# Kernel tuning notes

Measured on AMD Instinct MI355X. Metric: run time of the kernel, lower is better.

Reference implementation:

```python
import jax, jax.numpy as jnp
import numpy as np

B, S, D, H = 4, 8192, 512, 8
HD = D // H  # head_dim = 64


def setup_inputs() -> dict:
    key0 = jax.random.key(0)
    ks = jax.random.split(key0, 8)
    scale_in = (2.0 / (D + 3 * D)) ** 0.5  # xavier_uniform-ish std
    scale_out = (2.0 / (D + D)) ** 0.5
    return {
        "query": jax.random.normal(ks[0], (B, S, D), dtype=jnp.float32),
        "key": jax.random.normal(ks[1], (B, S, D), dtype=jnp.float32),
        "value": jax.random.normal(ks[2], (B, S, D), dtype=jnp.float32),
        "key_padding_mask": jax.random.bernoulli(ks[3], 0.1, (B, S)),  # True = ignore
        "in_proj_weight": jax.random.normal(ks[4], (3 * D, D), dtype=jnp.float32) * scale_in,
        "in_proj_bias": jnp.zeros((3 * D,), dtype=jnp.float32),
        "out_proj_weight": jax.random.normal(ks[5], (D, D), dtype=jnp.float32) * scale_out,
        "out_proj_bias": jnp.zeros((D,), dtype=jnp.float32),
    }


def _phi(x):
    # ELU+1 feature map (strictly positive)
    return jax.nn.elu(x) + 1.0


def reference(query, key, value, key_padding_mask, in_proj_weight, in_proj_bias,
              out_proj_weight, out_proj_bias):
    # NB: the torch module projects q,k,v all from `query`; key/value args are unused.
    qkv = query @ in_proj_weight.T + in_proj_bias  # (B,S,3D)
    q, k, v = jnp.split(qkv, 3, axis=-1)
    # (B,S,D) -> (B,H,S,HD)
    def to_heads(x):
        return x.reshape(B, S, H, HD).transpose(0, 2, 1, 3)
    q = _phi(to_heads(q))
    k = _phi(to_heads(k))
    v = to_heads(v)
    mask = (~key_padding_mask).astype(q.dtype)[:, None, :, None]  # (B,1,S,1)
    k = k * mask
    v = v * mask
    kv = jnp.einsum('bhsd,bhse->bhde', k, v)          # (B,H,HD,HD)
    numerator = jnp.einsum('bhsd,bhde->bhse', q, kv)  # (B,H,S,HD)
    k_sum = k.sum(axis=2)                              # (B,H,HD)
    denominator = jnp.einsum('bhsd,bhd->bhs', q, k_sum)[..., None]
    denominator = jnp.maximum(denominator, 1e-6)
    attn_out = (numerator / denominator).transpose(0, 2, 1, 3).reshape(B, S, D)
    return attn_out @ out_proj_weight.T + out_proj_bias
```

## Files before the change

kernel.cpp:

```cpp
#include <hip/hip_runtime.h>
#include <cstddef>

#define B_   4
#define S_   8192
#define D_   512
#define H_   8
#define HD_  64
#define NROW (B_ * S_)
#define NQ   ((size_t)NROW * D_)

typedef __attribute__((ext_vector_type(4))) float  f32x4;
typedef __attribute__((ext_vector_type(8))) short  s16x8;
typedef __attribute__((ext_vector_type(4))) unsigned short u16x4;
typedef __attribute__((ext_vector_type(8))) unsigned short u16x8;

__device__ __forceinline__ float phi_f(float x) {
    return x > 0.0f ? x + 1.0f : expf(x);
}
__device__ __forceinline__ float bf2f(unsigned short u) {
    return __uint_as_float(((unsigned int)u) << 16);
}
__device__ __forceinline__ unsigned short f2bf(float f) {
    unsigned int u = __float_as_uint(f);
    u += 0x7fffu + ((u >> 16) & 1u);
    return (unsigned short)(u >> 16);
}

#define GLOBAL_AS(p) ((const __attribute__((address_space(1))) void*)(p))
#define LDS_AS(p)    ((__attribute__((address_space(3))) void*)(p))

__global__ void detect_mask(const unsigned char* __restrict__ m, int* __restrict__ flag) {
    __shared__ int sany;
    if (threadIdx.x == 0) sany = 0;
    __syncthreads();
    int any = 0;
    for (int i = 1 + 4 * (int)threadIdx.x; i < NROW; i += 4 * 256) any |= m[i];
    if (any) atomicOr(&sany, 1);
    __syncthreads();
    if (threadIdx.x == 0) *flag = sany ? 1 : 0;
}

__global__ __launch_bounds__(256) void convert_all(
    const float* __restrict__ q,  unsigned short* __restrict__ qb,
    const float* __restrict__ wi, unsigned short* __restrict__ wib,
    const float* __restrict__ wo, unsigned short* __restrict__ wob,
    const unsigned char* __restrict__ kpm, const int* __restrict__ flag,
    float* __restrict__ fmask)
{
    const size_t i = (size_t)blockIdx.x * 256 + threadIdx.x;
    {
        const float4 v = *(const float4*)&q[i * 4];
        u16x4 o; o.x = f2bf(v.x); o.y = f2bf(v.y); o.z = f2bf(v.z); o.w = f2bf(v.w);
        *(u16x4*)&qb[i * 4] = o;
    }
    if (i < 786432 / 4) {
        const float4 v = *(const float4*)&wi[i * 4];
        u16x4 o; o.x = f2bf(v.x); o.y = f2bf(v.y); o.z = f2bf(v.z); o.w = f2bf(v.w);
        *(u16x4*)&wib[i * 4] = o;
    }
    if (i < 262144 / 4) {
        const float4 v = *(const float4*)&wo[i * 4];
        u16x4 o; o.x = f2bf(v.x); o.y = f2bf(v.y); o.z = f2bf(v.z); o.w = f2bf(v.w);
        *(u16x4*)&wob[i * 4] = o;
    }
    if (i < NROW) {
        const bool ignore = (*flag) ? (kpm[i] != 0) : (((const int*)kpm)[i] != 0);
        fmask[i] = ignore ? 0.0f : 1.0f;
    }
}

__global__ __launch_bounds__(256) void gemm_mfma(
    const unsigned short* __restrict__ A,  int lda,
    const unsigned short* __restrict__ Bw, int ldb,
    const float* __restrict__ bias, int K, int mode,
    const float* __restrict__ fmask,
    unsigned short* __restrict__ Cq,
    unsigned short* __restrict__ Ck,
    unsigned short* __restrict__ Cv,
    float* __restrict__ Cout)
{
    __shared__ __align__(16) unsigned short As[128 * 32];
    __shared__ __align__(16) unsigned short Bs[128 * 32];
    __shared__ float fm[128];

    const int t    = threadIdx.x;
    const int lane = t & 63;
    const int wave = t >> 6;
    const int wm   = wave & 1;
    const int wn   = wave >> 1;

    const int nbx = gridDim.x;
    const int nwg = nbx * gridDim.y;
    int id = blockIdx.y * nbx + blockIdx.x;
    id = (id & 7) * (nwg >> 3) + (id >> 3);
    const int m0 = (id / nbx) * 128;
    const int n0 = (id % nbx) * 128;

    if (mode == 0 && t < 128) fm[t] = fmask[m0 + t];

    f32x4 acc[4][4] = {};

    const int sr = lane >> 2;
    const int sk = (lane & 3) * 8;

    for (int k0 = 0; k0 < K; k0 += 32) {
        __syncthreads();
        #pragma unroll
        for (int j = 0; j < 2; ++j) {
            const int row = wave * 32 + j * 16;
            const unsigned short* g = A + (size_t)(m0 + row + sr) * lda + k0 + sk;
            __builtin_amdgcn_global_load_lds(GLOBAL_AS(g), LDS_AS(&As[row * 32]), 16, 0, 0);
        }
        #pragma unroll
        for (int j = 0; j < 2; ++j) {
            const int row = wave * 32 + j * 16;
            const unsigned short* g = Bw + (size_t)(n0 + row + sr) * ldb + k0 + sk;
            __builtin_amdgcn_global_load_lds(GLOBAL_AS(g), LDS_AS(&Bs[row * 32]), 16, 0, 0);
        }
        __syncthreads();

        const int fr = lane & 15;
        const int fk = (lane >> 4) * 8;
        s16x8 af[4], bf[4];
        #pragma unroll
        for (int i = 0; i < 4; ++i)
            af[i] = *(const s16x8*)&As[(wm * 64 + i * 16 + fr) * 32 + fk];
        #pragma unroll
        for (int j = 0; j < 4; ++j)
            bf[j] = *(const s16x8*)&Bs[(wn * 64 + j * 16 + fr) * 32 + fk];
        #pragma unroll
        for (int i = 0; i < 4; ++i)
            #pragma unroll
            for (int j = 0; j < 4; ++j)
                acc[i][j] = __builtin_amdgcn_mfma_f32_16x16x32_bf16(af[i], bf[j], acc[i][j], 0, 0, 0);
    }

    const int col  = lane & 15;
    const int rowq = (lane >> 4) * 4;
    float bj[4];
    #pragma unroll
    for (int j = 0; j < 4; ++j) bj[j] = bias[n0 + wn * 64 + j * 16 + col];

    if (mode == 1) {
        #pragma unroll
        for (int i = 0; i < 4; ++i)
            #pragma unroll
            for (int r = 0; r < 4; ++r) {
                const int m = m0 + wm * 64 + i * 16 + rowq + r;
                #pragma unroll
                for (int j = 0; j < 4; ++j) {
                    const int n = n0 + wn * 64 + j * 16 + col;
                    Cout[(size_t)m * D_ + n] = acc[i][j][r] + bj[j];
                }
            }
    } else {
        const int region = n0 >> 9;
        unsigned short* Cb = region == 0 ? Cq : (region == 1 ? Ck : Cv);
        #pragma unroll
        for (int i = 0; i < 4; ++i)
            #pragma unroll
            for (int r = 0; r < 4; ++r) {
                const int ml = wm * 64 + i * 16 + rowq + r;
                const int m  = m0 + ml;
                const float mk = fm[ml];
                #pragma unroll
                for (int j = 0; j < 4; ++j) {
                    const int n  = (n0 & 511) + wn * 64 + j * 16 + col;
                    float v = acc[i][j][r] + bj[j];
                    if (region == 0)      v = phi_f(v);
                    else if (region == 1) v = phi_f(v) * mk;
                    else                  v = v * mk;
                    Cb[(size_t)m * D_ + n] = f2bf(v);
                }
            }
    }
}

__global__ __launch_bounds__(256) void kv_reduce(
    const unsigned short* __restrict__ kbuf,
    const unsigned short* __restrict__ vbuf,
    float* __restrict__ part_kv,
    float* __restrict__ part_ks)
{
    const int bh = blockIdx.x, chunk = blockIdx.y;
    const int b = bh >> 3, h = bh & 7;

    __shared__ __align__(16) float Ks[16][68];
    __shared__ __align__(16) float Vs[16][68];

    const int t    = threadIdx.x;
    const int wave = t >> 6;
    const int lane = t & 63;
    const int tx   = lane & 7;
    const int ty   = lane >> 3;

    const int sr = (t & 127) >> 3;
    const int sc = (t & 7) * 8;
    const unsigned short* src = (t < 128 ? kbuf : vbuf) + (size_t)b * S_ * D_ + h * HD_;
    float (*dst)[68] = (t < 128) ? Ks : Vs;

    float acc[8][8] = {};
    float ks[8] = {};
    const int s0 = chunk * (S_ / 16);

    for (int it = 0; it < S_ / 16; it += 16) {
        const size_t s = (size_t)(s0 + it + sr);
        const u16x8 x = *(const u16x8*)&src[s * D_ + sc];
        __syncthreads();
        float4 f0, f1;
        f0.x = bf2f(x[0]); f0.y = bf2f(x[1]); f0.z = bf2f(x[2]); f0.w = bf2f(x[3]);
        f1.x = bf2f(x[4]); f1.y = bf2f(x[5]); f1.z = bf2f(x[6]); f1.w = bf2f(x[7]);
        *(float4*)&dst[sr][sc]     = f0;
        *(float4*)&dst[sr][sc + 4] = f1;
        __syncthreads();
        #pragma unroll
        for (int ss0 = 0; ss0 < 4; ++ss0) {
            const int ss = wave + ss0 * 4;
            const float4 a0 = *(const float4*)&Ks[ss][ty * 8];
            const float4 a1 = *(const float4*)&Ks[ss][ty * 8 + 4];
            const float4 v0 = *(const float4*)&Vs[ss][tx * 8];
            const float4 v1 = *(const float4*)&Vs[ss][tx * 8 + 4];
            const float av[8] = {a0.x, a0.y, a0.z, a0.w, a1.x, a1.y, a1.z, a1.w};
            const float vv[8] = {v0.x, v0.y, v0.z, v0.w, v1.x, v1.y, v1.z, v1.w};
            #pragma unroll
            for (int i2 = 0; i2 < 8; ++i2)
                #pragma unroll
                for (int j2 = 0; j2 < 8; ++j2)
                    acc[i2][j2] += av[i2] * vv[j2];
            if (tx == 0) {
                #pragma unroll
                for (int i2 = 0; i2 < 8; ++i2) ks[i2] += av[i2];
            }
        }
    }

    const int p = bh * 64 + chunk * 4 + wave;
    float* pk = part_kv + (size_t)p * 4096;
    #pragma unroll
    for (int i2 = 0; i2 < 8; ++i2) {
        #pragma unroll
        for (int j4 = 0; j4 < 2; ++j4) {
            float4 o;
            o.x = acc[i2][j4 * 4 + 0]; o.y = acc[i2][j4 * 4 + 1];
            o.z = acc[i2][j4 * 4 + 2]; o.w = acc[i2][j4 * 4 + 3];
            *(float4*)&pk[(ty * 8 + i2) * 64 + tx * 8 + j4 * 4] = o;
        }
    }
    if (tx == 0) {
        float* ps = part_ks + (size_t)p * 64;
        #pragma unroll
        for (int i2 = 0; i2 < 8; ++i2) ps[ty * 8 + i2] = ks[i2];
    }
}

__global__ void kv_reduce2(const float* __restrict__ part_kv,
                           const float* __restrict__ part_ks,
                           unsigned short* __restrict__ kvT,
                           unsigned short* __restrict__ ksumb)
{
    const int i = blockIdx.x * 256 + threadIdx.x;
    if (i < 32 * 4096) {
        const int bh = i >> 12, de = i & 4095;
        const int d = de >> 6, e = de & 63;
        float s = 0.0f;
        #pragma unroll
        for (int c = 0; c < 64; ++c) s += part_kv[(size_t)(bh * 64 + c) * 4096 + de];
        kvT[bh * 4096 + e * 64 + d] = f2bf(s);
    }
    if (i < 32 * 64) {
        const int bh = i >> 6, e = i & 63;
        float s = 0.0f;
        #pragma unroll
        for (int c = 0; c < 64; ++c) s += part_ks[(size_t)(bh * 64 + c) * 64 + e];
        ksumb[i] = f2bf(s);
    }
}

__global__ __launch_bounds__(256) void apply_attn_mfma(
    const unsigned short* __restrict__ qphi,
    const unsigned short* __restrict__ kvT,
    const unsigned short* __restrict__ ksumb,
    unsigned short* __restrict__ attnb)
{
    const int bh = blockIdx.x;
    const int b  = bh >> 3, h = bh & 7;
    const int m0 = blockIdx.y * 128;

    const int t    = threadIdx.x;
    const int lane = t & 63;
    const int wave = t >> 6;
    const int fr   = lane & 15;
    const int fk   = (lane >> 4) * 8;
    const int row0 = m0 + wave * 32;

    const unsigned short* Ah = qphi + (size_t)(b * S_ + row0) * D_ + h * HD_;
    const unsigned short* Bh = kvT + bh * 4096;
    const unsigned short* Kh = ksumb + bh * 64;

    s16x8 af[2][2], bfr[2][4], bd[2];
    #pragma unroll
    for (int kc = 0; kc < 2; ++kc) {
        #pragma unroll
        for (int i = 0; i < 2; ++i)
            af[kc][i] = *(const s16x8*)&Ah[(size_t)(i * 16 + fr) * D_ + kc * 32 + fk];
        #pragma unroll
        for (int j = 0; j < 4; ++j)
            bfr[kc][j] = *(const s16x8*)&Bh[(j * 16 + fr) * 64 + kc * 32 + fk];
        bd[kc] = *(const s16x8*)&Kh[kc * 32 + fk];
    }

    f32x4 acc[2][4] = {};
    f32x4 accd[2] = {};
    #pragma unroll
    for (int kc = 0; kc < 2; ++kc)
        #pragma unroll
        for (int i = 0; i < 2; ++i) {
            #pragma unroll
            for (int j = 0; j < 4; ++j)
                acc[i][j] = __builtin_amdgcn_mfma_f32_16x16x32_bf16(af[kc][i], bfr[kc][j], acc[i][j], 0, 0, 0);
            accd[i] = __builtin_amdgcn_mfma_f32_16x16x32_bf16(af[kc][i], bd[kc], accd[i], 0, 0, 0);
        }

    const int rq = (lane >> 4) * 4;
    #pragma unroll
    for (int i = 0; i < 2; ++i)
        #pragma unroll
        for (int r = 0; r < 4; ++r) {
            const float inv = 1.0f / fmaxf(accd[i][r], 1e-6f);
            const size_t row = (size_t)(b * S_ + row0 + i * 16 + rq + r);
            #pragma unroll
            for (int j = 0; j < 4; ++j)
                attnb[row * D_ + h * HD_ + j * 16 + fr] = f2bf(acc[i][j][r] * inv);
        }
}

extern "C" void kernel_launch(void* const* d_in, const int* in_sizes, int n_in,
                              void* d_out, int out_size, void* d_ws, size_t ws_size,
                              hipStream_t stream)
{
    const float* query       = (const float*)d_in[0];
    const unsigned char* kpm = (const unsigned char*)d_in[3];
    const float* w_in        = (const float*)d_in[4];
    const float* b_in        = (const float*)d_in[5];
    const float* w_out       = (const float*)d_in[6];
    const float* b_out       = (const float*)d_in[7];
    float* out = (float*)d_out;

    unsigned short* qb    = (unsigned short*)d_ws;
    unsigned short* qphi  = qb    + NQ;
    unsigned short* kpb   = qphi  + NQ;
    unsigned short* vmb   = kpb   + NQ;
    unsigned short* wib   = vmb   + NQ;
    unsigned short* wob   = wib   + 1536 * 512;
    float* fmask   = (float*)(wob + 512 * 512);
    float* part_kv = fmask + NROW;
    float* part_ks = part_kv + (size_t)2048 * 4096;
    unsigned short* kvTb  = (unsigned short*)(part_ks + 2048 * 64);
    unsigned short* ksumb = kvTb + 32 * 4096;
    int*   flag    = (int*)(ksumb + 32 * 64);

    hipLaunchKernelGGL(detect_mask, dim3(1), dim3(256), 0, stream, kpm, flag);
    hipLaunchKernelGGL(convert_all, dim3(16384), dim3(256), 0, stream,
                       query, qb, w_in, wib, w_out, wob, kpm, flag, fmask);

    hipLaunchKernelGGL(gemm_mfma, dim3(1536 / 128, NROW / 128), dim3(256), 0, stream,
                       qb, D_, wib, D_, b_in, D_, 0, fmask,
                       qphi, kpb, vmb, (float*)nullptr);

    hipLaunchKernelGGL(kv_reduce, dim3(32, 16), dim3(256), 0, stream, kpb, vmb, part_kv, part_ks);
    hipLaunchKernelGGL(kv_reduce2, dim3(512), dim3(256), 0, stream,
                       part_kv, part_ks, kvTb, ksumb);

    hipLaunchKernelGGL(apply_attn_mfma, dim3(32, S_ / 128), dim3(256), 0, stream,
                       qphi, kvTb, ksumb, qb);

    hipLaunchKernelGGL(gemm_mfma, dim3(512 / 128, NROW / 128), dim3(256), 0, stream,
                       qb, D_, wob, D_, b_out, D_, 1, (const float*)nullptr,
                       (unsigned short*)nullptr, (unsigned short*)nullptr,
                       (unsigned short*)nullptr, out);
}
```

Measured before the change: 408.4 us.

## Double-buffer GEMM LDS tiles and XOR-swizzle layout to avoid bank conflicts

Adds two LDS buffers for the A and B tiles so the global-to-LDS load of the next K slice is issued before the MFMA work on the current slice, cutting one barrier per iteration. It also applies an XOR swizzle to the 8-element chunk column, both when loading and when reading fragments, to reduce LDS bank conflicts on the fragment reads. This doubles LDS use per block, which may lower occupancy, and the swizzle must match exactly between writer and reader.

```diff
diff --git a/kernel.cpp b/kernel.cpp
--- a/kernel.cpp
+++ b/kernel.cpp
@@ -79,8 +79,8 @@
     unsigned short* __restrict__ Cv,
     float* __restrict__ Cout)
 {
-    __shared__ __align__(16) unsigned short As[128 * 32];
-    __shared__ __align__(16) unsigned short Bs[128 * 32];
+    __shared__ __align__(16) unsigned short As[2][128 * 32];
+    __shared__ __align__(16) unsigned short Bs[2][128 * 32];
     __shared__ float fm[128];
 
     const int t    = threadIdx.x;
@@ -100,39 +100,64 @@
 
     f32x4 acc[4][4] = {};
 
-    const int sr = lane >> 2;
-    const int sk = (lane & 3) * 8;
-
-    for (int k0 = 0; k0 < K; k0 += 32) {
-        __syncthreads();
+    const int sr  = lane >> 2;
+    const int skc = (((lane & 3) ^ ((lane >> 3) & 3))) * 8;
+
+    const int nt = K >> 5;
+
+    {
         #pragma unroll
         for (int j = 0; j < 2; ++j) {
             const int row = wave * 32 + j * 16;
-            const unsigned short* g = A + (size_t)(m0 + row + sr) * lda + k0 + sk;
-            __builtin_amdgcn_global_load_lds(GLOBAL_AS(g), LDS_AS(&As[row * 32]), 16, 0, 0);
+            const unsigned short* g = A + (size_t)(m0 + row + sr) * lda + skc;
+            __builtin_amdgcn_global_load_lds(GLOBAL_AS(g), LDS_AS(&As[0][row * 32]), 16, 0, 0);
         }
         #pragma unroll
         for (int j = 0; j < 2; ++j) {
             const int row = wave * 32 + j * 16;
-            const unsigned short* g = Bw + (size_t)(n0 + row + sr) * ldb + k0 + sk;
-            __builtin_amdgcn_global_load_lds(GLOBAL_AS(g), LDS_AS(&Bs[row * 32]), 16, 0, 0);
+            const unsigned short* g = Bw + (size_t)(n0 + row + sr) * ldb + skc;
+            __builtin_amdgcn_global_load_lds(GLOBAL_AS(g), LDS_AS(&Bs[0][row * 32]), 16, 0, 0);
         }
         __syncthreads();
-
-        const int fr = lane & 15;
-        const int fk = (lane >> 4) * 8;
+    }
+
+    const int fr = lane & 15;
+    const int cn = lane >> 4;
+    const int fo = (cn ^ ((fr >> 1) & 3)) * 8;
+
+    for (int kt = 0; kt < nt; ++kt) {
+        const int cur = kt & 1;
+        if (kt + 1 < nt) {
+            const int nb = cur ^ 1;
+            const int kn = (kt + 1) << 5;
+            #pragma unroll
+            for (int j = 0; j < 2; ++j) {
+                const int row = wave * 32 + j * 16;
+                const unsigned short* g = A + (size_t)(m0 + row + sr) * lda + kn + skc;
+                __builtin_amdgcn_global_load_lds(GLOBAL_AS(g), LDS_AS(&As[nb][row * 32]), 16, 0, 0);
+            }
+            #pragma unroll
+            for (int j = 0; j < 2; ++j) {
+                const int row = wave * 32 + j * 16;
+                const unsigned short* g = Bw + (size_t)(n0 + row + sr) * ldb + kn + skc;
+                __builtin_amdgcn_global_load_lds(GLOBAL_AS(g), LDS_AS(&Bs[nb][row * 32]), 16, 0, 0);
+            }
+        }
+
         s16x8 af[4], bf[4];
         #pragma unroll
         for (int i = 0; i < 4; ++i)
-            af[i] = *(const s16x8*)&As[(wm * 64 + i * 16 + fr) * 32 + fk];
+            af[i] = *(const s16x8*)&As[cur][(wm * 64 + i * 16 + fr) * 32 + fo];
         #pragma unroll
         for (int j = 0; j < 4; ++j)
-            bf[j] = *(const s16x8*)&Bs[(wn * 64 + j * 16 + fr) * 32 + fk];
+            bf[j] = *(const s16x8*)&Bs[cur][(wn * 64 + j * 16 + fr) * 32 + fo];
         #pragma unroll
         for (int i = 0; i < 4; ++i)
             #pragma unroll
             for (int j = 0; j < 4; ++j)
                 acc[i][j] = __builtin_amdgcn_mfma_f32_16x16x32_bf16(af[i], bf[j], acc[i][j], 0, 0, 0);
+
+        __syncthreads();
     }
 
     const int col  = lane & 15;
```

After: 393.7 us. 3.6% less time.

## Triple-buffer GEMM LDS tiles with async prefetch and XOR-swizzled layout

Applied to the files above, without the earlier changes.

Replaces the single-buffered LDS staging in the MFMA GEMM with a three-stage ring buffer. Tiles are prefetched two k-steps ahead, and the loop uses vmcnt waits and a single barrier per iteration so global loads overlap MFMA work. The column chunk is XOR-swizzled on both the global-to-LDS write and the fragment reads to reduce LDS bank conflicts. This triples the LDS used for tiles, which may lower occupancy, and the single-barrier scheme relies on the three-buffer distance to avoid overwriting a tile still being read.

```diff
diff --git a/kernel.cpp b/kernel.cpp
--- a/kernel.cpp
+++ b/kernel.cpp
@@ -79,8 +79,8 @@
     unsigned short* __restrict__ Cv,
     float* __restrict__ Cout)
 {
-    __shared__ __align__(16) unsigned short As[128 * 32];
-    __shared__ __align__(16) unsigned short Bs[128 * 32];
+    __shared__ __align__(16) unsigned short As[3][128 * 32];
+    __shared__ __align__(16) unsigned short Bs[3][128 * 32];
     __shared__ float fm[128];
 
     const int t    = threadIdx.x;
@@ -100,40 +100,64 @@
 
     f32x4 acc[4][4] = {};
 
-    const int sr = lane >> 2;
-    const int sk = (lane & 3) * 8;
-
-    for (int k0 = 0; k0 < K; k0 += 32) {
-        __syncthreads();
-        #pragma unroll
-        for (int j = 0; j < 2; ++j) {
-            const int row = wave * 32 + j * 16;
-            const unsigned short* g = A + (size_t)(m0 + row + sr) * lda + k0 + sk;
-            __builtin_amdgcn_global_load_lds(GLOBAL_AS(g), LDS_AS(&As[row * 32]), 16, 0, 0);
+    const int sr  = lane >> 2;
+    const int skc = (((lane & 3) ^ ((lane >> 3) & 3))) * 8;
+
+    const int nt = K >> 5;
+
+    #define STAGE(kt_, buf_)                                                            \
+        do {                                                                            \
+            const int k0_ = (kt_) << 5;                                                 \
+            _Pragma("unroll")                                                           \
+            for (int j = 0; j < 2; ++j) {                                               \
+                const int row = wave * 32 + j * 16;                                     \
+                const unsigned short* g = A + (size_t)(m0 + row + sr) * lda + k0_ + skc;\
+                __builtin_amdgcn_global_load_lds(GLOBAL_AS(g),                          \
+                    LDS_AS(&As[(buf_)][row * 32]), 16, 0, 0);                           \
+            }                                                                           \
+            _Pragma("unroll")                                                           \
+            for (int j = 0; j < 2; ++j) {                                               \
+                const int row = wave * 32 + j * 16;                                     \
+                const unsigned short* g = Bw + (size_t)(n0 + row + sr) * ldb + k0_ + skc;\
+                __builtin_amdgcn_global_load_lds(GLOBAL_AS(g),                          \
+                    LDS_AS(&Bs[(buf_)][row * 32]), 16, 0, 0);                           \
+            }                                                                           \
+        } while (0)
+
+    STAGE(0, 0);
+    STAGE(1, 1);
+
+    const int fr = lane & 15;
+    const int cn = lane >> 4;
+    const int fo = (cn ^ ((fr >> 1) & 3)) * 8;
+
+    int cur = 0;
+    for (int kt = 0; kt < nt; ++kt) {
+        if (kt + 1 < nt) asm volatile("s_waitcnt vmcnt(4)" ::: "memory");
+        else             asm volatile("s_waitcnt vmcnt(0)" ::: "memory");
+        __builtin_amdgcn_s_barrier();
+
+        if (kt + 2 < nt) {
+            int nb = cur + 2; if (nb >= 3) nb -= 3;
+            STAGE(kt + 2, nb);
         }
-        #pragma unroll
-        for (int j = 0; j < 2; ++j) {
-            const int row = wave * 32 + j * 16;
-            const unsigned short* g = Bw + (size_t)(n0 + row + sr) * ldb + k0 + sk;
-            __builtin_amdgcn_global_load_lds(GLOBAL_AS(g), LDS_AS(&Bs[row * 32]), 16, 0, 0);
-        }
-        __syncthreads();
-
-        const int fr = lane & 15;
-        const int fk = (lane >> 4) * 8;
+
         s16x8 af[4], bf[4];
         #pragma unroll
         for (int i = 0; i < 4; ++i)
-            af[i] = *(const s16x8*)&As[(wm * 64 + i * 16 + fr) * 32 + fk];
+            af[i] = *(const s16x8*)&As[cur][(wm * 64 + i * 16 + fr) * 32 + fo];
         #pragma unroll
         for (int j = 0; j < 4; ++j)
-            bf[j] = *(const s16x8*)&Bs[(wn * 64 + j * 16 + fr) * 32 + fk];
+            bf[j] = *(const s16x8*)&Bs[cur][(wn * 64 + j * 16 + fr) * 32 + fo];
         #pragma unroll
         for (int i = 0; i < 4; ++i)
             #pragma unroll
             for (int j = 0; j < 4; ++j)
                 acc[i][j] = __builtin_amdgcn_mfma_f32_16x16x32_bf16(af[i], bf[j], acc[i][j], 0, 0, 0);
-    }
+
+        if (++cur == 3) cur = 0;
+    }
+    #undef STAGE
 
     const int col  = lane & 15;
     const int rowq = (lane >> 4) * 4;
```

New measurement: 396.6 us. 2.9% less time.

## Replace 128x128 GEMM with 256x256 double-buffered ping-pong MFMA kernel

Applied to the files above, without the earlier changes.

Replaces the GEMM used for the QKV input projection and the output projection with a 256x256-tile, 512-thread kernel. It double-buffers 64-wide K tiles in LDS, uses an XOR-swizzled LDS layout to avoid bank conflicts, and splits each K tile into phases that interleave global-to-LDS loads with MFMA quadrants, using explicit barriers, waitcnts and setprio. The goal is to hide memory latency and raise MFMA utilisation by reusing larger tiles. In exchange it uses more LDS and registers, and the grid becomes much smaller (the out-projection launches only 256 workgroups), which may underfill the GPU.

```diff
diff --git a/kernel.cpp b/kernel.cpp
--- a/kernel.cpp
+++ b/kernel.cpp
@@ -69,7 +69,7 @@
     }
 }
 
-__global__ __launch_bounds__(256) void gemm_mfma(
+__global__ __launch_bounds__(512, 2) void gemm_mfma256(
     const unsigned short* __restrict__ A,  int lda,
     const unsigned short* __restrict__ Bw, int ldb,
     const float* __restrict__ bias, int K, int mode,
@@ -79,94 +79,186 @@
     unsigned short* __restrict__ Cv,
     float* __restrict__ Cout)
 {
-    __shared__ __align__(16) unsigned short As[128 * 32];
-    __shared__ __align__(16) unsigned short Bs[128 * 32];
-    __shared__ float fm[128];
+    __shared__ __align__(16) unsigned short As[2][256][64];
+    __shared__ __align__(16) unsigned short Bs[2][256][64];
+    __shared__ float fm[256];
 
     const int t    = threadIdx.x;
     const int lane = t & 63;
-    const int wave = t >> 6;
-    const int wm   = wave & 1;
-    const int wn   = wave >> 1;
+    const int wv   = t >> 6;
+    const int wm   = wv >> 2;
+    const int wn   = wv & 3;
 
     const int nbx = gridDim.x;
     const int nwg = nbx * gridDim.y;
     int id = blockIdx.y * nbx + blockIdx.x;
     id = (id & 7) * (nwg >> 3) + (id >> 3);
-    const int m0 = (id / nbx) * 128;
-    const int n0 = (id % nbx) * 128;
-
-    if (mode == 0 && t < 128) fm[t] = fmask[m0 + t];
-
-    f32x4 acc[4][4] = {};
-
-    const int sr = lane >> 2;
-    const int sk = (lane & 3) * 8;
-
-    for (int k0 = 0; k0 < K; k0 += 32) {
-        __syncthreads();
-        #pragma unroll
-        for (int j = 0; j < 2; ++j) {
-            const int row = wave * 32 + j * 16;
-            const unsigned short* g = A + (size_t)(m0 + row + sr) * lda + k0 + sk;
-            __builtin_amdgcn_global_load_lds(GLOBAL_AS(g), LDS_AS(&As[row * 32]), 16, 0, 0);
-        }
-        #pragma unroll
-        for (int j = 0; j < 2; ++j) {
-            const int row = wave * 32 + j * 16;
-            const unsigned short* g = Bw + (size_t)(n0 + row + sr) * ldb + k0 + sk;
-            __builtin_amdgcn_global_load_lds(GLOBAL_AS(g), LDS_AS(&Bs[row * 32]), 16, 0, 0);
-        }
-        __syncthreads();
-
-        const int fr = lane & 15;
-        const int fk = (lane >> 4) * 8;
-        s16x8 af[4], bf[4];
-        #pragma unroll
-        for (int i = 0; i < 4; ++i)
-            af[i] = *(const s16x8*)&As[(wm * 64 + i * 16 + fr) * 32 + fk];
-        #pragma unroll
-        for (int j = 0; j < 4; ++j)
-            bf[j] = *(const s16x8*)&Bs[(wn * 64 + j * 16 + fr) * 32 + fk];
-        #pragma unroll
-        for (int i = 0; i < 4; ++i)
-            #pragma unroll
-            for (int j = 0; j < 4; ++j)
-                acc[i][j] = __builtin_amdgcn_mfma_f32_16x16x32_bf16(af[i], bf[j], acc[i][j], 0, 0, 0);
-    }
-
-    const int col  = lane & 15;
-    const int rowq = (lane >> 4) * 4;
+    const int m0 = (id / nbx) * 256;
+    const int n0 = (id % nbx) * 256;
+
+    if (mode == 0 && t < 256) fm[t] = fmask[m0 + t];
+
+    f32x4 acc[8][4] = {};
+
+    const int srow  = lane >> 3;
+    const int clog8 = ((lane & 7) ^ (srow & 7)) * 8;
+    const int fr  = lane & 15;
+    const int fr7 = fr & 7;
+    const int cn  = lane >> 4;
+
+    const int niter = K >> 7;
+
+    #define SB0() __builtin_amdgcn_sched_barrier(0)
+
+    #define STAGE_HALF(DST, SRC, ld, org, tt, h)                                     \
+        do {                                                                         \
+            _Pragma("unroll")                                                        \
+            for (int l_ = 0; l_ < 2; ++l_) {                                         \
+                const int rl_ = (h) * 128 + wv * 16 + l_ * 8;                        \
+                const unsigned short* g_ = (SRC)                                     \
+                    + (size_t)((org) + rl_ + srow) * (ld) + ((tt) << 6) + clog8;     \
+                __builtin_amdgcn_global_load_lds(GLOBAL_AS(g_),                      \
+                    LDS_AS(&DST[rl_][0]), 16, 0, 0);                                 \
+            }                                                                        \
+        } while (0)
+
+    #define LOAD_AF(u, mh)                                                           \
+        _Pragma("unroll")                                                            \
+        for (int ii = 0; ii < 4; ++ii)                                               \
+            _Pragma("unroll")                                                        \
+            for (int w2 = 0; w2 < 2; ++w2)                                           \
+                a[ii][w2] = *(const s16x8*)&As[u][(((mh)*4 + ii)*2 + wm)*16 + fr]    \
+                                               [((w2*4 + cn) ^ fr7) * 8];
+
+    #define LOAD_BF(u, nh)                                                           \
+        _Pragma("unroll")                                                            \
+        for (int jj = 0; jj < 2; ++jj)                                               \
+            _Pragma("unroll")                                                        \
+            for (int w2 = 0; w2 < 2; ++w2)                                           \
+                b[jj][w2] = *(const s16x8*)&Bs[u][(((nh)*2 + jj)*4 + wn)*16 + fr]    \
+                                               [((w2*4 + cn) ^ fr7) * 8];
+
+    #define MFMA_Q(mh, nh)                                                           \
+        __builtin_amdgcn_s_setprio(1);                                               \
+        _Pragma("unroll")                                                            \
+        for (int w2 = 0; w2 < 2; ++w2)                                               \
+            _Pragma("unroll")                                                        \
+            for (int ii = 0; ii < 4; ++ii)                                           \
+                _Pragma("unroll")                                                    \
+                for (int jj = 0; jj < 2; ++jj)                                       \
+                    acc[(mh)*4 + ii][(nh)*2 + jj] =                                  \
+                        __builtin_amdgcn_mfma_f32_16x16x32_bf16(                     \
+                            a[ii][w2], b[jj][w2], acc[(mh)*4 + ii][(nh)*2 + jj],     \
+                            0, 0, 0);                                                \
+        __builtin_amdgcn_s_setprio(0);
+
+    #define PHASE_CORE(mh, nh, VWAIT)                                                \
+        SB0();                                                                       \
+        __builtin_amdgcn_s_barrier();                                                \
+        asm volatile("s_waitcnt lgkmcnt(0)" ::: "memory");                           \
+        SB0();                                                                       \
+        MFMA_Q(mh, nh)                                                               \
+        SB0();                                                                       \
+        VWAIT                                                                        \
+        __builtin_amdgcn_s_barrier();                                                \
+        SB0();
+
+    #define VW_NONE
+    #define VW_4  asm volatile("s_waitcnt vmcnt(4)" ::: "memory");
+    #define VW_0  asm volatile("s_waitcnt vmcnt(0)" ::: "memory");
+
+    s16x8 a[4][2], b[2][2];
+
+    STAGE_HALF(As[0], A,  lda, m0, 0, 0);
+    STAGE_HALF(As[0], A,  lda, m0, 0, 1);
+    STAGE_HALF(Bs[0], Bw, ldb, n0, 0, 0);
+    STAGE_HALF(Bs[0], Bw, ldb, n0, 0, 1);
+    STAGE_HALF(As[1], A,  lda, m0, 1, 0);
+    STAGE_HALF(Bs[1], Bw, ldb, n0, 1, 1);
+    SB0();
+    asm volatile("s_waitcnt vmcnt(4)" ::: "memory");
+    __builtin_amdgcn_s_barrier();
+    SB0();
+
+    for (int i = 0; i < niter; ++i) {
+        const int more = (i < niter - 1);
+
+        LOAD_AF(0, 0) LOAD_BF(0, 0)
+        STAGE_HALF(As[1], A, lda, m0, 2*i + 1, 1);
+        PHASE_CORE(0, 0, VW_NONE)
+
+        LOAD_BF(0, 1)
+        STAGE_HALF(Bs[1], Bw, ldb, n0, 2*i + 1, 0);
+        PHASE_CORE(0, 1, VW_NONE)
+
+        LOAD_AF(0, 1)
+        if (more) STAGE_HALF(As[0], A, lda, m0, 2*i + 2, 0);
+        PHASE_CORE(1, 1, VW_NONE)
+
+        LOAD_BF(0, 0)
+        if (more) STAGE_HALF(Bs[0], Bw, ldb, n0, 2*i + 2, 1);
+        if (more) { PHASE_CORE(1, 0, VW_4) }
+        else      { PHASE_CORE(1, 0, VW_0) }
+
+        LOAD_AF(1, 0) LOAD_BF(1, 0)
+        if (more) STAGE_HALF(As[0], A, lda, m0, 2*i + 2, 1);
+        PHASE_CORE(0, 0, VW_NONE)
+
+        LOAD_BF(1, 1)
+        if (more) STAGE_HALF(Bs[0], Bw, ldb, n0, 2*i + 2, 0);
+        PHASE_CORE(0, 1, VW_NONE)
+
+        LOAD_AF(1, 1)
+        if (more) STAGE_HALF(As[1], A, lda, m0, 2*i + 3, 0);
+        PHASE_CORE(1, 1, VW_NONE)
+
+        LOAD_BF(1, 0)
+        if (more) STAGE_HALF(Bs[1], Bw, ldb, n0, 2*i + 3, 1);
+        PHASE_CORE(1, 0, VW_4)
+    }
+
+    #undef STAGE_HALF
+    #undef LOAD_AF
+    #undef LOAD_BF
+    #undef MFMA_Q
+    #undef PHASE_CORE
+    #undef VW_NONE
+    #undef VW_4
+    #undef VW_0
+    #undef SB0
+
+    const int colf = lane & 15;
+    const int rq   = (lane >> 4) * 4;
     float bj[4];
     #pragma unroll
-    for (int j = 0; j < 4; ++j) bj[j] = bias[n0 + wn * 64 + j * 16 + col];
+    for (int j = 0; j < 4; ++j) bj[j] = bias[n0 + (j*4 + wn)*16 + colf];
 
     if (mode == 1) {
         #pragma unroll
-        for (int i = 0; i < 4; ++i)
+        for (int ig = 0; ig < 8; ++ig)
             #pragma unroll
             for (int r = 0; r < 4; ++r) {
-                const int m = m0 + wm * 64 + i * 16 + rowq + r;
+                const int m = m0 + (ig*2 + wm)*16 + rq + r;
                 #pragma unroll
                 for (int j = 0; j < 4; ++j) {
-                    const int n = n0 + wn * 64 + j * 16 + col;
-                    Cout[(size_t)m * D_ + n] = acc[i][j][r] + bj[j];
+                    const int n = n0 + (j*4 + wn)*16 + colf;
+                    Cout[(size_t)m * D_ + n] = acc[ig][j][r] + bj[j];
                 }
             }
     } else {
         const int region = n0 >> 9;
         unsigned short* Cb = region == 0 ? Cq : (region == 1 ? Ck : Cv);
         #pragma unroll
-        for (int i = 0; i < 4; ++i)
+        for (int ig = 0; ig < 8; ++ig)
             #pragma unroll
             for (int r = 0; r < 4; ++r) {
-                const int ml = wm * 64 + i * 16 + rowq + r;
+                const int ml = (ig*2 + wm)*16 + rq + r;
                 const int m  = m0 + ml;
                 const float mk = fm[ml];
                 #pragma unroll
                 for (int j = 0; j < 4; ++j) {
-                    const int n  = (n0 & 511) + wn * 64 + j * 16 + col;
-                    float v = acc[i][j][r] + bj[j];
+                    const int n = (n0 & 511) + (j*4 + wn)*16 + colf;
+                    float v = acc[ig][j][r] + bj[j];
                     if (region == 0)      v = phi_f(v);
                     else if (region == 1) v = phi_f(v) * mk;
                     else                  v = v * mk;
@@ -363,7 +455,7 @@
     hipLaunchKernelGGL(convert_all, dim3(16384), dim3(256), 0, stream,
                        query, qb, w_in, wib, w_out, wob, kpm, flag, fmask);
 
-    hipLaunchKernelGGL(gemm_mfma, dim3(1536 / 128, NROW / 128), dim3(256), 0, stream,
+    hipLaunchKernelGGL(gemm_mfma256, dim3(1536 / 256, NROW / 256), dim3(512), 0, stream,
                        qb, D_, wib, D_, b_in, D_, 0, fmask,
                        qphi, kpb, vmb, (float*)nullptr);
 
@@ -374,7 +466,7 @@
     hipLaunchKernelGGL(apply_attn_mfma, dim3(32, S_ / 128), dim3(256), 0, stream,
                        qphi, kvTb, ksumb, qb);
 
-    hipLaunchKernelGGL(gemm_mfma, dim3(512 / 128, NROW / 128), dim3(256), 0, stream,
+    hipLaunchKernelGGL(gemm_mfma256, dim3(512 / 256, NROW / 256), dim3(512), 0, stream,
                        qb, D_, wob, D_, b_out, D_, 1, (const float*)nullptr,
                        (unsigned short*)nullptr, (unsigned short*)nullptr,
                        (unsigned short*)nullptr, out);
```

Result: no change. 406.2 us (-0.6%).
